# Optimization experiments

Measured on AMD Instinct MI355X. Metric: run time of the kernel, lower is better.

## Reference

```python
import jax, jax.numpy as jnp
import numpy as np

B, N, M = 2, 2048, 2048
D = 1024          # query_dim == context_dim == inner_dim
H, DH = 16, 64    # heads, dim_head
SCALE = DH ** -0.5


def setup_inputs() -> dict:
    key = jax.random.key(0)
    ks = jax.random.split(key, 7)
    s = 0.02
    return {
        "x": jax.random.normal(ks[0], (B, N, D), jnp.float32),
        "context": jax.random.normal(ks[1], (B, M, D), jnp.float32),
        "Wq": jax.random.normal(ks[2], (D, H * DH), jnp.float32) * s,
        "Wk": jax.random.normal(ks[3], (D, H * DH), jnp.float32) * s,
        "Wv": jax.random.normal(ks[4], (D, H * DH), jnp.float32) * s,
        "Wo": jax.random.normal(ks[5], (H * DH, D), jnp.float32) * s,
        "bo": jax.random.normal(ks[6], (D,), jnp.float32) * s,
    }


def reference(x, context, Wq, Wk, Wv, Wo, bo):
    # Linear projections (bias-free, as in to_q/to_k/to_v)
    q = (x @ Wq).reshape(B, N, H, DH)        # [B,N,H,DH]
    k = (context @ Wk).reshape(B, M, H, DH)  # [B,M,H,DH]
    v = (context @ Wv).reshape(B, M, H, DH)
    # QK^T * scale, softmax over keys, then AV
    sim = jnp.einsum('bnhd,bmhd->bhnm', q, k) * SCALE  # [B,H,N,M]
    attn = jax.nn.softmax(sim, axis=-1)
    out = jnp.einsum('bhnm,bmhd->bnhd', attn, v)       # [B,N,H,DH]
    out = out.reshape(B, N, H * DH)
    return out @ Wo + bo  # to_out Linear; dropout=0 is identity
```

## Files before the change

### kernel.cpp

```cpp
#include <hip/hip_runtime.h>

#define B_  2
#define N_  2048
#define M_  2048
#define D_  1024
#define H_  16
#define DH_ 64

typedef __bf16 bf16x8 __attribute__((ext_vector_type(8)));
typedef __bf16 bf16x4 __attribute__((ext_vector_type(4)));
typedef short  short4v __attribute__((ext_vector_type(4)));
typedef float  f32x4  __attribute__((ext_vector_type(4)));
typedef unsigned int u32x4v __attribute__((ext_vector_type(4)));

#define GAS(p) ((__attribute__((address_space(1))) void*)(p))
#define LAS(p) ((__attribute__((address_space(3))) void*)(p))

#define QPRESCALE 0.18033688011112042f

__device__ __forceinline__ unsigned short f2bf(float f) {
    unsigned int u = __builtin_bit_cast(unsigned int, f);
    u += 0x7fffu + ((u >> 16) & 1u);
    return (unsigned short)(u >> 16);
}

__device__ __forceinline__ unsigned cvtpkbf(float a, float b) {
    unsigned r;
    asm("v_cvt_pk_bf16_f32 %0, %1, %2" : "=v"(r) : "v"(a), "v"(b));
    return r;
}

__global__ __launch_bounds__(256) void prep(
    const float* __restrict__ x, const float* __restrict__ ctx,
    const float* __restrict__ Wq, const float* __restrict__ Wk,
    const float* __restrict__ Wv, const float* __restrict__ Wo,
    unsigned short* __restrict__ xb, unsigned short* __restrict__ cb,
    unsigned short* __restrict__ WTbase)
{
    if (blockIdx.z == 4) {
        int blk = blockIdx.y * 32 + blockIdx.x;
        int stride = 1024 * 256;
        for (int i = blk * 256 + threadIdx.x; i < 2097152; i += stride) {
            const float4* src; unsigned short* dst; int j;
            if (i < 1048576) { src = (const float4*)x;   dst = xb; j = i; }
            else             { src = (const float4*)ctx; dst = cb; j = i - 1048576; }
            float4 v = src[j];
            ushort4 o = make_ushort4(f2bf(v.x), f2bf(v.y), f2bf(v.z), f2bf(v.w));
            *(ushort4*)(dst + 4*j) = o;
        }
        return;
    }
    const float* W = (blockIdx.z == 0) ? Wq : (blockIdx.z == 1) ? Wk
                    : (blockIdx.z == 2) ? Wv : Wo;
    unsigned short* WT = WTbase + (size_t)blockIdx.z * 1048576;
    __shared__ unsigned short t[32][33];
    int tx = threadIdx.x & 31, ty8 = threadIdx.x >> 5;
    int c = blockIdx.x * 32 + tx;
#pragma unroll
    for (int i = 0; i < 4; ++i) {
        int r = blockIdx.y * 32 + i*8 + ty8;
        t[i*8 + ty8][tx] = f2bf(W[(size_t)r * 1024 + c]);
    }
    __syncthreads();
    int c2 = blockIdx.y * 32 + tx;
#pragma unroll
    for (int i = 0; i < 4; ++i) {
        int r2 = blockIdx.x * 32 + i*8 + ty8;
        WT[(size_t)r2 * 1024 + c2] = t[tx][i*8 + ty8];
    }
}

__global__ __launch_bounds__(256) void gemm128(
    const unsigned short* __restrict__ xb,
    const unsigned short* __restrict__ cb,
    const unsigned short* __restrict__ wT,
    const unsigned short* __restrict__ aoA,
    unsigned short* __restrict__ qkv_out,
    const float* __restrict__ bo,
    float* __restrict__ outF,
    int base_mode)
{
    __shared__ __align__(16) unsigned short As[2][128*32];
    __shared__ __align__(16) unsigned short Bs[2][128*32];

    const int lin = (blockIdx.z * 8 + blockIdx.y) * 32 + blockIdx.x;
    const int idx = lin >> 3;
    const int p = (lin & 7) * 3 + (idx >> 5);
    const int mode = base_mode + (p >> 3);
    const int ytile = p & 7, xtile = idx & 31;

    const unsigned short* Amat;
    const unsigned short* Bt;
    if (mode == 0)      { Amat = wT;               Bt = xb; }
    else if (mode == 1) { Amat = wT + 1048576;     Bt = cb; }
    else                { Amat = cb;               Bt = wT + 2*1048576; }

    const int tid = threadIdx.x;
    const int w = tid >> 6, l = tid & 63;
    const int quad = l >> 4, l16 = l & 15;
    const int wm = w & 1, wn = w >> 1;
    int row0, col0;
    if (mode == 2) { row0 = xtile * 128; col0 = ytile * 128; }
    else           { row0 = ytile * 128; col0 = xtile * 128; }

    f32x4 acc[4][4];
#pragma unroll
    for (int i = 0; i < 4; ++i)
#pragma unroll
        for (int j = 0; j < 4; ++j) acc[i][j] = (f32x4){0.f, 0.f, 0.f, 0.f};

    for (int k0 = 0; k0 < 1024; k0 += 64) {
        __syncthreads();
#pragma unroll
        for (int h = 0; h < 2; ++h) {
#pragma unroll
            for (int i = 0; i < 2; ++i) {
                int s = i*256 + w*64 + l;
                int m = s >> 2, c = s & 3;
                int cs = c ^ ((m >> 1) & 3);
                __builtin_amdgcn_global_load_lds(
                    GAS(Amat + (size_t)(row0 + m)*1024 + k0 + h*32 + cs*8),
                    LAS(As[h] + (i*256 + w*64)*8), 16, 0, 0);
                __builtin_amdgcn_global_load_lds(
                    GAS(Bt + (size_t)(col0 + m)*1024 + k0 + h*32 + cs*8),
                    LAS(Bs[h] + (i*256 + w*64)*8), 16, 0, 0);
            }
        }
        __syncthreads();

#pragma unroll
        for (int h = 0; h < 2; ++h) {
            bf16x8 af[4], bfr[4];
#pragma unroll
            for (int mt = 0; mt < 4; ++mt) {
                int m = wm*64 + mt*16 + l16;
                af[mt] = *reinterpret_cast<const bf16x8*>(As[h] + m*32 + (quad ^ ((m >> 1) & 3))*8);
                int n = wn*64 + mt*16 + l16;
                bfr[mt] = *reinterpret_cast<const bf16x8*>(Bs[h] + n*32 + (quad ^ ((n >> 1) & 3))*8);
            }
#pragma unroll
            for (int mt = 0; mt < 4; ++mt)
#pragma unroll
                for (int nt = 0; nt < 4; ++nt)
                    acc[mt][nt] = __builtin_amdgcn_mfma_f32_16x16x32_bf16(
                        af[mt], bfr[nt], acc[mt][nt], 0, 0, 0);
        }
    }

    if (mode == 2) {
#pragma unroll
        for (int mt = 0; mt < 4; ++mt) {
            int gr = row0 + wm*64 + mt*16 + quad*4;
            int b = gr >> 11, nidx = gr & 2047;
#pragma unroll
            for (int nt = 0; nt < 4; ++nt) {
                int col = col0 + wn*64 + nt*16 + l16;
                int h = col >> 6, d = col & 63;
                ushort4 pk = make_ushort4(f2bf(acc[mt][nt][0]), f2bf(acc[mt][nt][1]),
                                          f2bf(acc[mt][nt][2]), f2bf(acc[mt][nt][3]));
                *(ushort4*)(qkv_out + (size_t)2*4194304
                            + (size_t)((b*16 + h)*64 + d)*2048 + nidx) = pk;
            }
        }
    } else {
        const float qs = (mode == 0) ? QPRESCALE : 1.0f;
        unsigned short* obase = qkv_out + (size_t)mode*4194304;
#pragma unroll
        for (int nt = 0; nt < 4; ++nt) {
            int n = col0 + wn*64 + nt*16 + l16;
            int b = n >> 11, nidx = n & 2047;
#pragma unroll
            for (int mt = 0; mt < 4; ++mt) {
                int c = row0 + wm*64 + mt*16 + quad*4;
                int h = c >> 6, d = c & 63;
                ushort4 pkv = make_ushort4(
                    f2bf(acc[mt][nt][0] * qs), f2bf(acc[mt][nt][1] * qs),
                    f2bf(acc[mt][nt][2] * qs), f2bf(acc[mt][nt][3] * qs));
                *(ushort4*)(obase + (size_t)((b*16 + h)*2048 + nidx)*64 + d) = pkv;
            }
        }
    }
}

__global__ __launch_bounds__(256) void gemm_out(
    const unsigned short* __restrict__ woT,
    const unsigned short* __restrict__ aoA,
    const float* __restrict__ bo,
    float* __restrict__ outF)
{
    __shared__ __align__(16) unsigned short As[2][64*32];
    __shared__ __align__(16) unsigned short Bs[2][128*32];

    const int tid = threadIdx.x;
    const int w = tid >> 6, l = tid & 63;
    const int quad = l >> 4, l16 = l & 15;
    const int lin = blockIdx.y * 32 + blockIdx.x;
    const int idx = lin >> 3;
    const int row0 = ((lin & 7) * 2 + (idx >> 5)) * 64;
    const int col0 = (idx & 31) * 128;

    f32x4 acc[4][2];
#pragma unroll
    for (int i = 0; i < 4; ++i)
#pragma unroll
        for (int j = 0; j < 2; ++j) acc[i][j] = (f32x4){0.f, 0.f, 0.f, 0.f};

    for (int k0 = 0; k0 < 1024; k0 += 64) {
        __syncthreads();
#pragma unroll
        for (int h = 0; h < 2; ++h) {
            {
                int m = tid >> 2, c = tid & 3;
                int cs = c ^ ((m >> 1) & 3);
                __builtin_amdgcn_global_load_lds(
                    GAS(woT + (size_t)(row0 + m)*1024 + k0 + h*32 + cs*8),
                    LAS(As[h] + (w*64)*8), 16, 0, 0);
            }
#pragma unroll
            for (int i = 0; i < 2; ++i) {
                int s = i*256 + tid;
                int m = s >> 2, c = s & 3;
                int cs = c ^ ((m >> 1) & 3);
                __builtin_amdgcn_global_load_lds(
                    GAS(aoA + (size_t)(col0 + m)*1024 + k0 + h*32 + cs*8),
                    LAS(Bs[h] + (i*256 + w*64)*8), 16, 0, 0);
            }
        }
        __syncthreads();

#pragma unroll
        for (int h = 0; h < 2; ++h) {
            bf16x8 af[4], bfr[2];
#pragma unroll
            for (int mt = 0; mt < 4; ++mt) {
                int m = mt*16 + l16;
                af[mt] = *reinterpret_cast<const bf16x8*>(As[h] + m*32 + (quad ^ ((m >> 1) & 3))*8);
            }
#pragma unroll
            for (int nt = 0; nt < 2; ++nt) {
                int n = w*32 + nt*16 + l16;
                bfr[nt] = *reinterpret_cast<const bf16x8*>(Bs[h] + n*32 + (quad ^ ((n >> 1) & 3))*8);
            }
#pragma unroll
            for (int mt = 0; mt < 4; ++mt)
#pragma unroll
                for (int nt = 0; nt < 2; ++nt)
                    acc[mt][nt] = __builtin_amdgcn_mfma_f32_16x16x32_bf16(
                        af[mt], bfr[nt], acc[mt][nt], 0, 0, 0);
        }
    }

#pragma unroll
    for (int mt = 0; mt < 4; ++mt) {
        int c = row0 + mt*16 + quad*4;
        float4 bv = *(const float4*)(bo + c);
#pragma unroll
        for (int nt = 0; nt < 2; ++nt) {
            int n = col0 + w*32 + nt*16 + l16;
            float4 ov = make_float4(acc[mt][nt][0] + bv.x, acc[mt][nt][1] + bv.y,
                                    acc[mt][nt][2] + bv.z, acc[mt][nt][3] + bv.w);
            *(float4*)(outF + (size_t)n*1024 + c) = ov;
        }
    }
}

__global__ __launch_bounds__(256, 2) void flash_attn(
    const unsigned short* __restrict__ qw,
    const unsigned short* __restrict__ kw,
    const unsigned short* __restrict__ vtw,
    unsigned short* __restrict__ ao)
{
    __shared__ __align__(16) unsigned short Tile[2][9216];

    const int tid = threadIdx.x;
    const int w = tid >> 6, l = tid & 63;
    const int quad = l >> 4, l16 = l & 15;
    const int lin = (blockIdx.z * 16 + blockIdx.y) * 16 + blockIdx.x;
    const int bh = (lin & 7) * 4 + (lin >> 7);
    const int qt = (lin >> 3) & 15;
    const int qh = w & 1, kvh = w >> 1;
    const int q0 = qt * 128 + qh * 64;

    int goff[5];
#pragma unroll
    for (int i = 0; i < 5; ++i) {
        int n = i*256 + w*64 + l;
        int m = (n < 576) ? n : n - 576;
        int row = m / 9, c = m % 9;  if (c > 7) c = 7;
        goff[i] = (n < 576) ? row*64 + c*8 : row*2048 + c*8;
    }
    const unsigned short* kbase = kw + (size_t)bh*131072;
    const unsigned short* vbase = vtw + (size_t)bh*131072;

    bf16x8 qf[4][2];
#pragma unroll
    for (int qg = 0; qg < 4; ++qg)
#pragma unroll
        for (int s = 0; s < 2; ++s)
            qf[qg][s] = *reinterpret_cast<const bf16x8*>(
                qw + (size_t)(bh*2048 + q0 + qg*16 + l16)*64 + s*32 + quad*8);

    f32x4 accO[4][4];
#pragma unroll
    for (int qg = 0; qg < 4; ++qg)
#pragma unroll
        for (int td = 0; td < 4; ++td) accO[qg][td] = (f32x4){0.f, 0.f, 0.f, 0.f};
    float lpart[4] = {0.f, 0.f, 0.f, 0.f};

    const f32x4 zz = (f32x4){0.f, 0.f, 0.f, 0.f};

    {
#pragma unroll
        for (int i = 0; i < 4; ++i) {
            const unsigned short* bp = (i*4 + w < 9) ? kbase : vbase;
            __builtin_amdgcn_global_load_lds(GAS(bp + goff[i]),
                LAS(&Tile[0][(i*256 + w*64)*8]), 16, 0, 0);
        }
        if (w < 2)
            __builtin_amdgcn_global_load_lds(GAS(vbase + goff[4]),
                LAS(&Tile[0][(1024 + w*64)*8]), 16, 0, 0);
    }

    for (int it = 0; it < 32; ++it) {
        __syncthreads();
        const int cur = it & 1;

        if (it + 1 < 32) {
            const unsigned short* kp = kbase + (it+1)*4096;
            const unsigned short* vp = vbase + (it+1)*64;
#pragma unroll
            for (int i = 0; i < 4; ++i) {
                const unsigned short* bp = (i*4 + w < 9) ? kp : vp;
                __builtin_amdgcn_global_load_lds(GAS(bp + goff[i]),
                    LAS(&Tile[cur^1][(i*256 + w*64)*8]), 16, 0, 0);
            }
            if (w < 2)
                __builtin_amdgcn_global_load_lds(GAS(vp + goff[4]),
                    LAS(&Tile[cur^1][(1024 + w*64)*8]), 16, 0, 0);
        }

        const unsigned short* Ks = &Tile[cur][0];
        const unsigned short* Vs = &Tile[cur][4608];

        f32x4 sac[4][2];
        __builtin_amdgcn_s_setprio(1);
#pragma unroll
        for (int t = 0; t < 2; ++t) {
            const unsigned short* krow = Ks + (kvh*32 + t*16 + l16)*72 + quad*8;
            bf16x8 kf0 = *reinterpret_cast<const bf16x8*>(krow);
            bf16x8 kf1 = *reinterpret_cast<const bf16x8*>(krow + 32);
#pragma unroll
            for (int qg = 0; qg < 4; ++qg) {
                sac[qg][t] = __builtin_amdgcn_mfma_f32_16x16x32_bf16(kf0, qf[qg][0], zz, 0, 0, 0);
                sac[qg][t] = __builtin_amdgcn_mfma_f32_16x16x32_bf16(kf1, qf[qg][1], sac[qg][t], 0, 0, 0);
            }
        }
        __builtin_amdgcn_s_setprio(0);

        u32x4v pB[4];
#pragma unroll
        for (int qg = 0; qg < 4; ++qg) {
            float pe0 = __builtin_amdgcn_exp2f(sac[qg][0][0]);
            float pe1 = __builtin_amdgcn_exp2f(sac[qg][0][1]);
            float pe2 = __builtin_amdgcn_exp2f(sac[qg][0][2]);
            float pe3 = __builtin_amdgcn_exp2f(sac[qg][0][3]);
            float po0 = __builtin_amdgcn_exp2f(sac[qg][1][0]);
            float po1 = __builtin_amdgcn_exp2f(sac[qg][1][1]);
            float po2 = __builtin_amdgcn_exp2f(sac[qg][1][2]);
            float po3 = __builtin_amdgcn_exp2f(sac[qg][1][3]);
            lpart[qg] += ((pe0 + po0) + (pe1 + po1)) + ((pe2 + po2) + (pe3 + po3));
            unsigned b0 = cvtpkbf(pe0, pe1), b1 = cvtpkbf(pe2, pe3);
            unsigned b2 = cvtpkbf(po0, po1), b3 = cvtpkbf(po2, po3);
            asm("v_permlane32_swap_b32 %0, %1" : "+v"(b0), "+v"(b2));
            asm("v_permlane16_swap_b32 %0, %1" : "+v"(b0), "+v"(b2));
            asm("v_permlane32_swap_b32 %0, %1" : "+v"(b1), "+v"(b3));
            asm("v_permlane16_swap_b32 %0, %1" : "+v"(b1), "+v"(b3));
            pB[qg] = (u32x4v){b0, b1, b2, b3};
        }

        __builtin_amdgcn_s_setprio(1);
#pragma unroll
        for (int td = 0; td < 4; ++td) {
            bf16x8 vf = *reinterpret_cast<const bf16x8*>(
                Vs + (td*16 + l16)*72 + kvh*32 + quad*8);
#pragma unroll
            for (int qg = 0; qg < 4; ++qg)
                accO[qg][td] = __builtin_amdgcn_mfma_f32_16x16x32_bf16(
                    vf, __builtin_bit_cast(bf16x8, pB[qg]), accO[qg][td], 0, 0, 0);
        }
        __builtin_amdgcn_s_setprio(0);
    }

    float* xch = (float*)&Tile[0][0];
    __syncthreads();
    if (kvh == 1) {
        float* base = xch + (size_t)(qh*64 + l)*72;
#pragma unroll
        for (int qg = 0; qg < 4; ++qg)
#pragma unroll
            for (int td = 0; td < 4; ++td)
                *(f32x4*)(base + (qg*4 + td)*4) = accO[qg][td];
        *(f32x4*)(base + 64) = (f32x4){lpart[0], lpart[1], lpart[2], lpart[3]};
    }
    __syncthreads();
    if (kvh == 0) {
        const float* base = xch + (size_t)(qh*64 + l)*72;
#pragma unroll
        for (int qg = 0; qg < 4; ++qg)
#pragma unroll
            for (int td = 0; td < 4; ++td)
                accO[qg][td] += *(const f32x4*)(base + (qg*4 + td)*4);
        f32x4 lp2 = *(const f32x4*)(base + 64);
        lpart[0] += lp2[0]; lpart[1] += lp2[1];
        lpart[2] += lp2[2]; lpart[3] += lp2[3];

        const int bb = bh >> 4, hh = bh & 15;
#pragma unroll
        for (int qg = 0; qg < 4; ++qg) {
            float s = lpart[qg];
            s += __shfl_xor(s, 16);
            s += __shfl_xor(s, 32);
            float inv = 1.f / s;
            const size_t rowbase =
                (size_t)(bb*2048 + q0 + qg*16 + l16)*1024 + hh*64;
#pragma unroll
            for (int td = 0; td < 4; ++td)
#pragma unroll
                for (int r = 0; r < 4; ++r)
                    ao[rowbase + td*16 + quad*4 + r] = f2bf(accO[qg][td][r] * inv);
        }
    }
}

extern "C" void kernel_launch(void* const* d_in, const int* in_sizes, int n_in,
                              void* d_out, int out_size, void* d_ws, size_t ws_size,
                              hipStream_t stream)
{
    const float* x   = (const float*)d_in[0];
    const float* ctx = (const float*)d_in[1];
    const float* Wq  = (const float*)d_in[2];
    const float* Wk  = (const float*)d_in[3];
    const float* Wv  = (const float*)d_in[4];
    const float* Wo  = (const float*)d_in[5];
    const float* bo  = (const float*)d_in[6];
    float* out = (float*)d_out;

    unsigned short* ws  = (unsigned short*)d_ws;
    unsigned short* xb  = ws;
    unsigned short* cb  = ws + 4194304;
    unsigned short* wT  = ws + 8388608;
    unsigned short* qkv = ws + 12582912;
    unsigned short* ao  = ws;

    prep<<<dim3(32, 32, 5), dim3(256), 0, stream>>>(x, ctx, Wq, Wk, Wv, Wo, xb, cb, wT);
    gemm128<<<dim3(32, 8, 3), dim3(256), 0, stream>>>(xb, cb, wT, ao, qkv, bo, out, 0);
    flash_attn<<<dim3(16, 16, 2), dim3(256), 0, stream>>>(qkv, qkv + 4194304, qkv + 8388608, ao);
    gemm_out<<<dim3(32, 16), dim3(256), 0, stream>>>(wT + 3*1048576, ao, bo, out);
}
```

Measured before the change: 200.6 us.

## Double-buffer LDS tiles in projection GEMMs to overlap loads with MFMA

Both the QKV projection GEMM and the output projection GEMM now use the two LDS buffers as a ping-pong pipeline. The next 32-wide K slice is issued into one buffer while MFMAs run on the other, so each iteration needs one barrier instead of two. This hides global-to-LDS latency behind compute. The cost is half the K depth per barrier interval and twice as many loop iterations.

```diff
diff --git a/kernel.cpp b/kernel.cpp
--- a/kernel.cpp
+++ b/kernel.cpp
@@ -109,42 +109,44 @@
 #pragma unroll
         for (int j = 0; j < 4; ++j) acc[i][j] = (f32x4){0.f, 0.f, 0.f, 0.f};
 
-    for (int k0 = 0; k0 < 1024; k0 += 64) {
+    auto stage = [&](int k0, int b) {
+#pragma unroll
+        for (int i = 0; i < 2; ++i) {
+            int s = i*256 + w*64 + l;
+            int m = s >> 2, c = s & 3;
+            int cs = c ^ ((m >> 1) & 3);
+            __builtin_amdgcn_global_load_lds(
+                GAS(Amat + (size_t)(row0 + m)*1024 + k0 + cs*8),
+                LAS(As[b] + (i*256 + w*64)*8), 16, 0, 0);
+            __builtin_amdgcn_global_load_lds(
+                GAS(Bt + (size_t)(col0 + m)*1024 + k0 + cs*8),
+                LAS(Bs[b] + (i*256 + w*64)*8), 16, 0, 0);
+        }
+    };
+
+    stage(0, 0);
+    __syncthreads();
+
+    for (int t = 0; t < 32; ++t) {
+        const int cur = t & 1;
+        if (t + 1 < 32) stage((t + 1) * 32, cur ^ 1);
+
+        bf16x8 af[4], bfr[4];
+#pragma unroll
+        for (int mt = 0; mt < 4; ++mt) {
+            int m = wm*64 + mt*16 + l16;
+            af[mt] = *reinterpret_cast<const bf16x8*>(As[cur] + m*32 + (quad ^ ((m >> 1) & 3))*8);
+            int n = wn*64 + mt*16 + l16;
+            bfr[mt] = *reinterpret_cast<const bf16x8*>(Bs[cur] + n*32 + (quad ^ ((n >> 1) & 3))*8);
+        }
+#pragma unroll
+        for (int mt = 0; mt < 4; ++mt)
+#pragma unroll
+            for (int nt = 0; nt < 4; ++nt)
+                acc[mt][nt] = __builtin_amdgcn_mfma_f32_16x16x32_bf16(
+                    af[mt], bfr[nt], acc[mt][nt], 0, 0, 0);
+
         __syncthreads();
-#pragma unroll
-        for (int h = 0; h < 2; ++h) {
-#pragma unroll
-            for (int i = 0; i < 2; ++i) {
-                int s = i*256 + w*64 + l;
-                int m = s >> 2, c = s & 3;
-                int cs = c ^ ((m >> 1) & 3);
-                __builtin_amdgcn_global_load_lds(
-                    GAS(Amat + (size_t)(row0 + m)*1024 + k0 + h*32 + cs*8),
-                    LAS(As[h] + (i*256 + w*64)*8), 16, 0, 0);
-                __builtin_amdgcn_global_load_lds(
-                    GAS(Bt + (size_t)(col0 + m)*1024 + k0 + h*32 + cs*8),
-                    LAS(Bs[h] + (i*256 + w*64)*8), 16, 0, 0);
-            }
-        }
-        __syncthreads();
-
-#pragma unroll
-        for (int h = 0; h < 2; ++h) {
-            bf16x8 af[4], bfr[4];
-#pragma unroll
-            for (int mt = 0; mt < 4; ++mt) {
-                int m = wm*64 + mt*16 + l16;
-                af[mt] = *reinterpret_cast<const bf16x8*>(As[h] + m*32 + (quad ^ ((m >> 1) & 3))*8);
-                int n = wn*64 + mt*16 + l16;
-                bfr[mt] = *reinterpret_cast<const bf16x8*>(Bs[h] + n*32 + (quad ^ ((n >> 1) & 3))*8);
-            }
-#pragma unroll
-            for (int mt = 0; mt < 4; ++mt)
-#pragma unroll
-                for (int nt = 0; nt < 4; ++nt)
-                    acc[mt][nt] = __builtin_amdgcn_mfma_f32_16x16x32_bf16(
-                        af[mt], bfr[nt], acc[mt][nt], 0, 0, 0);
-        }
     }
 
     if (mode == 2) {
@@ -205,49 +207,51 @@
 #pragma unroll
         for (int j = 0; j < 2; ++j) acc[i][j] = (f32x4){0.f, 0.f, 0.f, 0.f};
 
-    for (int k0 = 0; k0 < 1024; k0 += 64) {
+    auto stage = [&](int k0, int b) {
+        {
+            int m = tid >> 2, c = tid & 3;
+            int cs = c ^ ((m >> 1) & 3);
+            __builtin_amdgcn_global_load_lds(
+                GAS(woT + (size_t)(row0 + m)*1024 + k0 + cs*8),
+                LAS(As[b] + (w*64)*8), 16, 0, 0);
+        }
+#pragma unroll
+        for (int i = 0; i < 2; ++i) {
+            int s = i*256 + tid;
+            int m = s >> 2, c = s & 3;
+            int cs = c ^ ((m >> 1) & 3);
+            __builtin_amdgcn_global_load_lds(
+                GAS(aoA + (size_t)(col0 + m)*1024 + k0 + cs*8),
+                LAS(Bs[b] + (i*256 + w*64)*8), 16, 0, 0);
+        }
+    };
+
+    stage(0, 0);
+    __syncthreads();
+
+    for (int t = 0; t < 32; ++t) {
+        const int cur = t & 1;
+        if (t + 1 < 32) stage((t + 1) * 32, cur ^ 1);
+
+        bf16x8 af[4], bfr[2];
+#pragma unroll
+        for (int mt = 0; mt < 4; ++mt) {
+            int m = mt*16 + l16;
+            af[mt] = *reinterpret_cast<const bf16x8*>(As[cur] + m*32 + (quad ^ ((m >> 1) & 3))*8);
+        }
+#pragma unroll
+        for (int nt = 0; nt < 2; ++nt) {
+            int n = w*32 + nt*16 + l16;
+            bfr[nt] = *reinterpret_cast<const bf16x8*>(Bs[cur] + n*32 + (quad ^ ((n >> 1) & 3))*8);
+        }
+#pragma unroll
+        for (int mt = 0; mt < 4; ++mt)
+#pragma unroll
+            for (int nt = 0; nt < 2; ++nt)
+                acc[mt][nt] = __builtin_amdgcn_mfma_f32_16x16x32_bf16(
+                    af[mt], bfr[nt], acc[mt][nt], 0, 0, 0);
+
         __syncthreads();
-#pragma unroll
-        for (int h = 0; h < 2; ++h) {
-            {
-                int m = tid >> 2, c = tid & 3;
-                int cs = c ^ ((m >> 1) & 3);
-                __builtin_amdgcn_global_load_lds(
-                    GAS(woT + (size_t)(row0 + m)*1024 + k0 + h*32 + cs*8),
-                    LAS(As[h] + (w*64)*8), 16, 0, 0);
-            }
-#pragma unroll
-            for (int i = 0; i < 2; ++i) {
-                int s = i*256 + tid;
-                int m = s >> 2, c = s & 3;
-                int cs = c ^ ((m >> 1) & 3);
-                __builtin_amdgcn_global_load_lds(
-                    GAS(aoA + (size_t)(col0 + m)*1024 + k0 + h*32 + cs*8),
-                    LAS(Bs[h] + (i*256 + w*64)*8), 16, 0, 0);
-            }
-        }
-        __syncthreads();
-
-#pragma unroll
-        for (int h = 0; h < 2; ++h) {
-            bf16x8 af[4], bfr[2];
-#pragma unroll
-            for (int mt = 0; mt < 4; ++mt) {
-                int m = mt*16 + l16;
-                af[mt] = *reinterpret_cast<const bf16x8*>(As[h] + m*32 + (quad ^ ((m >> 1) & 3))*8);
-            }
-#pragma unroll
-            for (int nt = 0; nt < 2; ++nt) {
-                int n = w*32 + nt*16 + l16;
-                bfr[nt] = *reinterpret_cast<const bf16x8*>(Bs[h] + n*32 + (quad ^ ((n >> 1) & 3))*8);
-            }
-#pragma unroll
-            for (int mt = 0; mt < 4; ++mt)
-#pragma unroll
-                for (int nt = 0; nt < 2; ++nt)
-                    acc[mt][nt] = __builtin_amdgcn_mfma_f32_16x16x32_bf16(
-                        af[mt], bfr[nt], acc[mt][nt], 0, 0, 0);
-        }
     }
 
 #pragma unroll
```

Result: slower. 209.7 us (+4.5%).
